# Kernel optimization log

Measured on AMD Instinct MI355X. Metric: run time of the kernel, lower is better.

The kernel has to match this reference:

```python
import jax, jax.numpy as jnp
import numpy as np

STRIDE = 1
PAD = 1
EXTENT = 3  # kernel footprint (ceil of max tap offset), 3x3 tap grid


def setup_inputs() -> dict:
    key = jax.random.key(0)
    k1, k2 = jax.random.split(key)
    B, Cin, H, W = 8, 64, 128, 128
    Cout, K = 64, 9
    x = jax.random.normal(k1, (B, Cin, H, W), dtype=jnp.float32)
    # per-tap weights, one scalar weight per (out_ch, in_ch, tap) -- op formula is 'x * w'
    weights = jax.random.normal(k2, (Cout, Cin, K), dtype=jnp.float32) * 0.05
    # 3x3 integer grid shifted by +0.4 -> non-integer offsets => bilinear (sub-pixel) gather
    base = jnp.stack(jnp.meshgrid(jnp.arange(3.0), jnp.arange(3.0), indexing='ij'), -1).reshape(9, 2)
    tap_offsets = (base + 0.4).astype(jnp.float32)  # [K, 2] (dy, dx)
    return {"x": x, "weights": weights, "tap_offsets": tap_offsets}


def _bilinear_tap(xp, dy, dx, H_out, W_out):
    # Gather xp at (oy*stride + dy, ox*stride + dx) with separable bilinear interp.
    Hp, Wp = xp.shape[-2], xp.shape[-1]
    y = jnp.arange(H_out, dtype=xp.dtype) * STRIDE + dy
    xc = jnp.arange(W_out, dtype=xp.dtype) * STRIDE + dx
    y0 = jnp.floor(y)
    x0 = jnp.floor(xc)
    fy = (y - y0)[None, None, :, None]
    fx = (xc - x0)[None, None, None, :]
    y0i = jnp.clip(y0.astype(jnp.int32), 0, Hp - 1)
    y1i = jnp.clip(y0.astype(jnp.int32) + 1, 0, Hp - 1)
    x0i = jnp.clip(x0.astype(jnp.int32), 0, Wp - 1)
    x1i = jnp.clip(x0.astype(jnp.int32) + 1, 0, Wp - 1)
    # interp rows first: [B, C, H_out, Wp]
    ry = xp[:, :, y0i, :] * (1.0 - fy) + xp[:, :, y1i, :] * fy
    # then columns: [B, C, H_out, W_out]
    return ry[:, :, :, x0i] * (1.0 - fx) + ry[:, :, :, x1i] * fx


def reference(x, weights, tap_offsets):
    B, Cin, H, W = x.shape
    K = weights.shape[-1]
    xp = jnp.pad(x, ((0, 0), (0, 0), (PAD, PAD), (PAD, PAD)))
    H_out = (H + 2 * PAD - EXTENT) // STRIDE + 1
    W_out = (W + 2 * PAD - EXTENT) // STRIDE + 1
    # gather all taps (loop over small fixed K=9, each fully vectorized over B,C,H,W)
    taps = [_bilinear_tap(xp, tap_offsets[k, 0], tap_offsets[k, 1], H_out, W_out)
            for k in range(K)]
    g = jnp.stack(taps, 0)  # [K, B, Cin, H_out, W_out]
    # per-tap op 'x * w', accumulated over taps and input channels
    return jnp.einsum('kbiyx,oik->boyx', g, weights)  # [B, Cout, H_out, W_out]
```

## Files before the change

kernel.cpp:

```cpp
#include <hip/hip_runtime.h>


#define CIN   64
#define COUT  64
#define HH    128
#define WW    128

typedef __attribute__((ext_vector_type(8))) short bf16x8;
typedef __attribute__((ext_vector_type(4))) float f32x4;
typedef __attribute__((ext_vector_type(4))) unsigned int u32x4;

__device__ __forceinline__ unsigned short f2bf(float f) {
  unsigned int u = __float_as_uint(f);
  u = (u + 0x7fffu + ((u >> 16) & 1u)) >> 16;
  return (unsigned short)u;
}

__global__ void make_wb(const float* __restrict__ wgt,
                        const float* __restrict__ off,
                        unsigned short* __restrict__ wb2)
{
  int id = blockIdx.x * 64 + threadIdx.x;
  int o = id >> 6, c = id & 63;
  float W16[16];
  #pragma unroll
  for (int i = 0; i < 16; ++i) W16[i] = 0.f;
  for (int k = 0; k < 9; ++k) {
    float dy = off[2*k], dx = off[2*k+1];
    float fyf = floorf(dy), fxf = floorf(dx);
    int   iy = (int)fyf,   ix = (int)fxf;
    float fy = dy - fyf,   fx = dx - fxf;
    float wk = wgt[(o*CIN + c)*9 + k];
    W16[(iy  )*4 + ix  ] += wk * (1.f-fy)*(1.f-fx);
    W16[(iy  )*4 + ix+1] += wk * (1.f-fy)*fx;
    W16[(iy+1)*4 + ix  ] += wk * fy*(1.f-fx);
    W16[(iy+1)*4 + ix+1] += wk * fy*fx;
  }
  int p = c >> 5, q = (c >> 3) & 3, j = c & 7;
  int n = o >> 4, m15 = o & 15;
  int lanei = q*16 + m15;
  for (int rs = 0; rs < 16; ++rs)
    wb2[(size_t)(((p*16 + rs)*4 + n)*64 + lanei)*8 + j] = f2bf(W16[rs]);
}

__global__ __launch_bounds__(128, 2)
void conv_mfma(const float* __restrict__ x,
               const unsigned short* __restrict__ wb2,
               float* __restrict__ out)
{
  __shared__ unsigned short tile[4 * 132 * 32];

  const int wg  = blockIdx.x;
  const int xcd = wg & 7;
  const int i8  = wg >> 3;
  const int b   = i8 >> 4;
  const int y0  = xcd * 16 + (i8 & 15);
  const int t    = threadIdx.x;
  const int wave = t >> 6;
  const int lane = t & 63;
  const int m15  = lane & 15;
  const int q    = lane >> 4;

  f32x4 acc[4][4];
  #pragma unroll
  for (int mi = 0; mi < 4; ++mi)
    #pragma unroll
    for (int n = 0; n < 4; ++n)
      acc[mi][n] = (f32x4){0.f, 0.f, 0.f, 0.f};

  #pragma unroll
  for (int p = 0; p < 2; ++p) {
    if (p) __syncthreads();

    if (p == 0) {
      int row = t >> 5, rem = t & 31;
      int csel = rem >> 3;
      int col  = (csel == 0) ? 0 : (128 + csel);
      int w8   = rem & 7;
      *(unsigned long long*)&tile[(row*132 + col)*32 + w8*4] = 0ull;
    }

    #pragma unroll 4
    for (int it = 0; it < 16; ++it) {
      int g     = it*2 + wave;
      int row   = g >> 3;
      int rem   = g & 7;
      int chunk = rem >> 1;
      int xh    = rem & 1;
      int px    = xh*64 + lane;
      int gy    = y0 + row - 1;
      unsigned int pk[4];
      if ((unsigned)gy < (unsigned)HH) {
        const float* ps = x + ((size_t)((b*CIN + p*32 + chunk*8)*HH + gy))*WW + px;
        float v[8];
        #pragma unroll
        for (int cc = 0; cc < 8; ++cc) v[cc] = ps[(size_t)cc*HH*WW];
        #pragma unroll
        for (int i = 0; i < 4; ++i)
          pk[i] = (unsigned int)f2bf(v[2*i]) | ((unsigned int)f2bf(v[2*i+1]) << 16);
      } else {
        pk[0] = pk[1] = pk[2] = pk[3] = 0u;
      }
      int pos  = px + 1;
      int slot = (chunk + (pos >> 2)) & 3;
      *(u32x4*)&tile[((row*132 + pos)*4 + slot)*8] = *(u32x4*)pk;
    }
    __syncthreads();

    const unsigned short* wstream = wb2 + (size_t)p*16*4*512 + lane*8;
    #pragma unroll
    for (int rs = 0; rs < 16; ++rs) {
      const int r = rs >> 2, s = rs & 3;
      bf16x8 bfr[4];
      #pragma unroll
      for (int n = 0; n < 4; ++n)
        bfr[n] = *(const bf16x8*)(wstream + (rs*4 + n)*512);
      bf16x8 afr[4];
      #pragma unroll
      for (int mi = 0; mi < 4; ++mi) {
        int pos  = wave*64 + mi*16 + m15 + s;
        int slot = (q + (pos >> 2)) & 3;
        afr[mi] = *(const bf16x8*)(&tile[((r*132 + pos)*4 + slot)*8]);
      }
      #pragma unroll
      for (int mi = 0; mi < 4; ++mi)
        #pragma unroll
        for (int n = 0; n < 4; ++n)
          acc[mi][n] = __builtin_amdgcn_mfma_f32_16x16x32_bf16(afr[mi], bfr[n], acc[mi][n], 0, 0, 0);
    }
  }

  __syncthreads();
  float* epi = (float*)tile;
  #pragma unroll
  for (int mi = 0; mi < 4; ++mi)
    #pragma unroll
    for (int n = 0; n < 4; ++n) {
      int o  = n*16 + m15;
      int px = wave*64 + mi*16 + q*4;
      *(f32x4*)&epi[o*132 + px] = acc[mi][n];
    }
  __syncthreads();
  #pragma unroll
  for (int i = 0; i < 16; ++i) {
    int o  = i*4 + (t >> 5);
    int px = (t & 31) * 4;
    f32x4 v = *(const f32x4*)&epi[o*132 + px];
    *(f32x4*)&out[(((size_t)(b*COUT + o))*HH + y0)*WW + px] = v;
  }
}

extern "C" void kernel_launch(void* const* d_in, const int* in_sizes, int n_in,
                              void* d_out, int out_size, void* d_ws, size_t ws_size,
                              hipStream_t stream)
{
  const float* x   = (const float*)d_in[0];
  const float* wgt = (const float*)d_in[1];
  const float* off = (const float*)d_in[2];
  float* out = (float*)d_out;
  unsigned short* wb2 = (unsigned short*)d_ws;

  make_wb<<<64, 64, 0, stream>>>(wgt, off, wb2);
  conv_mfma<<<1024, 128, 0, stream>>>(x, wb2, out);
}
```

Measured before the change: 107.2 us.

## Pre-pack input to swizzled bf16 and stream tiles via global_load_lds

Adds a prep kernel that converts x once into a channel-packed, pre-swizzled bf16 layout in workspace, fused with the weight folding. The conv kernel then copies rows straight into LDS with global_load_lds 16-byte transfers, with no per-element fp32 loads, conversion or repacking. This removes the redundant 3x row re-reads and conversions done per workgroup. In exchange it adds an extra full pass over x (read fp32, write bf16) and a larger workspace footprint.

```diff
diff --git a/kernel.cpp b/kernel.cpp
--- a/kernel.cpp
+++ b/kernel.cpp
@@ -10,41 +10,76 @@
 typedef __attribute__((ext_vector_type(4))) float f32x4;
 typedef __attribute__((ext_vector_type(4))) unsigned int u32x4;
 
+#define GLOBAL_AS __attribute__((address_space(1)))
+#define LDS_AS    __attribute__((address_space(3)))
+
 __device__ __forceinline__ unsigned short f2bf(float f) {
   unsigned int u = __float_as_uint(f);
   u = (u + 0x7fffu + ((u >> 16) & 1u)) >> 16;
   return (unsigned short)u;
 }
 
-__global__ void make_wb(const float* __restrict__ wgt,
-                        const float* __restrict__ off,
-                        unsigned short* __restrict__ wb2)
+#define NREPACK 512
+#define NWB     16
+
+__global__ void prep(const float* __restrict__ x,
+                     const float* __restrict__ wgt,
+                     const float* __restrict__ off,
+                     unsigned short* __restrict__ xb,
+                     unsigned short* __restrict__ wb2)
 {
-  int id = blockIdx.x * 64 + threadIdx.x;
-  int o = id >> 6, c = id & 63;
-  float W16[16];
-  #pragma unroll
-  for (int i = 0; i < 16; ++i) W16[i] = 0.f;
-  for (int k = 0; k < 9; ++k) {
-    float dy = off[2*k], dx = off[2*k+1];
-    float fyf = floorf(dy), fxf = floorf(dx);
-    int   iy = (int)fyf,   ix = (int)fxf;
-    float fy = dy - fyf,   fx = dx - fxf;
-    float wk = wgt[(o*CIN + c)*9 + k];
-    W16[(iy  )*4 + ix  ] += wk * (1.f-fy)*(1.f-fx);
-    W16[(iy  )*4 + ix+1] += wk * (1.f-fy)*fx;
-    W16[(iy+1)*4 + ix  ] += wk * fy*(1.f-fx);
-    W16[(iy+1)*4 + ix+1] += wk * fy*fx;
+  if (blockIdx.x < NREPACK) {
+    int id = blockIdx.x * 256 + threadIdx.x;
+    int px = id & 127;
+    int y  = (id >> 7) & 127;
+    int b  = id >> 14;
+    int q4 = ((px + 1) >> 2) & 3;
+    unsigned int pk[2][16];
+    #pragma unroll
+    for (int i = 0; i < 16; ++i) { pk[0][i] = 0u; pk[1][i] = 0u; }
+    const float* src = x + ((size_t)b*CIN*HH + y)*WW + px;
+    #pragma unroll
+    for (int c = 0; c < CIN; ++c) {
+      float v = src[(size_t)c*HH*WW];
+      int p = c >> 5, chunk = (c >> 3) & 3, j = c & 7;
+      pk[p][chunk*4 + (j >> 1)] |= (unsigned int)f2bf(v) << ((j & 1) * 16);
+    }
+    #pragma unroll
+    for (int p = 0; p < 2; ++p) {
+      unsigned short* dst = xb + (((size_t)(b*2 + p)*HH + y)*WW + px)*32;
+      #pragma unroll
+      for (int chunk = 0; chunk < 4; ++chunk) {
+        int slot = (chunk + q4) & 3;
+        *(u32x4*)(dst + slot*8) = *(u32x4*)&pk[p][chunk*4];
+      }
+    }
+  } else {
+    int id = (blockIdx.x - NREPACK) * 256 + threadIdx.x;
+    int o = id >> 6, c = id & 63;
+    float W16[16];
+    #pragma unroll
+    for (int i = 0; i < 16; ++i) W16[i] = 0.f;
+    for (int k = 0; k < 9; ++k) {
+      float dy = off[2*k], dx = off[2*k+1];
+      float fyf = floorf(dy), fxf = floorf(dx);
+      int   iy = (int)fyf,   ix = (int)fxf;
+      float fy = dy - fyf,   fx = dx - fxf;
+      float wk = wgt[(o*CIN + c)*9 + k];
+      W16[(iy  )*4 + ix  ] += wk * (1.f-fy)*(1.f-fx);
+      W16[(iy  )*4 + ix+1] += wk * (1.f-fy)*fx;
+      W16[(iy+1)*4 + ix  ] += wk * fy*(1.f-fx);
+      W16[(iy+1)*4 + ix+1] += wk * fy*fx;
+    }
+    int p = c >> 5, q = (c >> 3) & 3, j = c & 7;
+    int n = o >> 4, m15 = o & 15;
+    int lanei = q*16 + m15;
+    for (int rs = 0; rs < 16; ++rs)
+      wb2[(size_t)(((p*16 + rs)*4 + n)*64 + lanei)*8 + j] = f2bf(W16[rs]);
   }
-  int p = c >> 5, q = (c >> 3) & 3, j = c & 7;
-  int n = o >> 4, m15 = o & 15;
-  int lanei = q*16 + m15;
-  for (int rs = 0; rs < 16; ++rs)
-    wb2[(size_t)(((p*16 + rs)*4 + n)*64 + lanei)*8 + j] = f2bf(W16[rs]);
 }
 
 __global__ __launch_bounds__(128, 2)
-void conv_mfma(const float* __restrict__ x,
+void conv_mfma(const unsigned short* __restrict__ xb,
                const unsigned short* __restrict__ wb2,
                float* __restrict__ out)
 {
@@ -68,6 +103,8 @@
     for (int n = 0; n < 4; ++n)
       acc[mi][n] = (f32x4){0.f, 0.f, 0.f, 0.f};
 
+  const size_t rowstride = (size_t)WW * 32;
+
   #pragma unroll
   for (int p = 0; p < 2; ++p) {
     if (p) __syncthreads();
@@ -80,30 +117,21 @@
       *(unsigned long long*)&tile[(row*132 + col)*32 + w8*4] = 0ull;
     }
 
-    #pragma unroll 4
+    const unsigned short* xbase = xb + (size_t)(b*2 + p)*HH*rowstride;
+    #pragma unroll
     for (int it = 0; it < 16; ++it) {
-      int g     = it*2 + wave;
-      int row   = g >> 3;
-      int rem   = g & 7;
-      int chunk = rem >> 1;
-      int xh    = rem & 1;
-      int px    = xh*64 + lane;
-      int gy    = y0 + row - 1;
-      unsigned int pk[4];
+      int g   = it*2 + wave;
+      int row = g >> 3;
+      int seg = g & 7;
+      int gy  = y0 + row - 1;
+      unsigned short* ldsdst = &tile[(row*132 + 1)*32 + seg*512];
       if ((unsigned)gy < (unsigned)HH) {
-        const float* ps = x + ((size_t)((b*CIN + p*32 + chunk*8)*HH + gy))*WW + px;
-        float v[8];
-        #pragma unroll
-        for (int cc = 0; cc < 8; ++cc) v[cc] = ps[(size_t)cc*HH*WW];
-        #pragma unroll
-        for (int i = 0; i < 4; ++i)
-          pk[i] = (unsigned int)f2bf(v[2*i]) | ((unsigned int)f2bf(v[2*i+1]) << 16);
-      } else {
-        pk[0] = pk[1] = pk[2] = pk[3] = 0u;
+        const unsigned short* src = xbase + (size_t)gy*rowstride + seg*512 + lane*8;
+        __builtin_amdgcn_global_load_lds((const GLOBAL_AS unsigned int*)src,
+                                         (LDS_AS unsigned int*)ldsdst, 16, 0, 0);
+      } else if (p == 0) {
+        *(u32x4*)(ldsdst + lane*8) = (u32x4){0u,0u,0u,0u};
       }
-      int pos  = px + 1;
-      int slot = (chunk + (pos >> 2)) & 3;
-      *(u32x4*)&tile[((row*132 + pos)*4 + slot)*8] = *(u32x4*)pk;
     }
     __syncthreads();
 
@@ -159,7 +187,8 @@
   const float* off = (const float*)d_in[2];
   float* out = (float*)d_out;
   unsigned short* wb2 = (unsigned short*)d_ws;
+  unsigned short* xb  = (unsigned short*)d_ws + 65536;
 
-  make_wb<<<64, 64, 0, stream>>>(wgt, off, wb2);
-  conv_mfma<<<1024, 128, 0, stream>>>(x, wb2, out);
+  prep<<<NREPACK + NWB, 256, 0, stream>>>(x, wgt, off, xb, wb2);
+  conv_mfma<<<1024, 128, 0, stream>>>(xb, wb2, out);
 }
```

Result: slower. 113.2 us (+5.7%).

## Compute two output rows per block with 4 waves sharing a 5-row input tile

Applied to the files above, without the earlier changes.

Each workgroup now produces two adjacent output rows with 256 threads: waves split by output row and by output-channel half, and they share a 5-row staged input tile instead of two separate 4-row tiles. This cuts redundant global loads and bf16 conversion of the overlapping input rows and halves the number of blocks. Halo rows are zeroed only on the first pass, and the epilogue writes the two rows in turn through shared memory using nontemporal stores. In exchange, per-wave accumulators grow to 8x2 MFMA tiles, the epilogue needs extra barriers, and half as many blocks may lower occupancy.

```diff
diff --git a/kernel.cpp b/kernel.cpp
--- a/kernel.cpp
+++ b/kernel.cpp
@@ -43,36 +43,39 @@
     wb2[(size_t)(((p*16 + rs)*4 + n)*64 + lanei)*8 + j] = f2bf(W16[rs]);
 }
 
-__global__ __launch_bounds__(128, 2)
+__global__ __launch_bounds__(256, 2)
 void conv_mfma(const float* __restrict__ x,
                const unsigned short* __restrict__ wb2,
                float* __restrict__ out)
 {
-  __shared__ unsigned short tile[4 * 132 * 32];
+  __shared__ unsigned short tile[5 * 132 * 32];
 
   const int wg  = blockIdx.x;
   const int xcd = wg & 7;
-  const int i8  = wg >> 3;
-  const int b   = i8 >> 4;
-  const int y0  = xcd * 16 + (i8 & 15);
-  const int t    = threadIdx.x;
-  const int wave = t >> 6;
-  const int lane = t & 63;
-  const int m15  = lane & 15;
-  const int q    = lane >> 4;
+  const int i   = wg >> 3;
+  const int b   = i >> 3;
+  const int ss  = i & 7;
+  const int y0  = xcd * 16 + ss * 2;
+  const int t     = threadIdx.x;
+  const int wave  = t >> 6;
+  const int lane  = t & 63;
+  const int m15   = lane & 15;
+  const int q     = lane >> 4;
+  const int yr    = wave >> 1;
+  const int ohalf = wave & 1;
 
-  f32x4 acc[4][4];
+  f32x4 acc[8][2];
   #pragma unroll
-  for (int mi = 0; mi < 4; ++mi)
+  for (int mi = 0; mi < 8; ++mi)
     #pragma unroll
-    for (int n = 0; n < 4; ++n)
-      acc[mi][n] = (f32x4){0.f, 0.f, 0.f, 0.f};
+    for (int nn = 0; nn < 2; ++nn)
+      acc[mi][nn] = (f32x4){0.f, 0.f, 0.f, 0.f};
 
   #pragma unroll
   for (int p = 0; p < 2; ++p) {
     if (p) __syncthreads();
 
-    if (p == 0) {
+    if (p == 0 && t < 160) {
       int row = t >> 5, rem = t & 31;
       int csel = rem >> 3;
       int col  = (csel == 0) ? 0 : (128 + csel);
@@ -80,73 +83,79 @@
       *(unsigned long long*)&tile[(row*132 + col)*32 + w8*4] = 0ull;
     }
 
-    #pragma unroll 4
-    for (int it = 0; it < 16; ++it) {
-      int g     = it*2 + wave;
+    #pragma unroll 2
+    for (int it = 0; it < 10; ++it) {
+      int g     = it*4 + wave;
       int row   = g >> 3;
       int rem   = g & 7;
       int chunk = rem >> 1;
       int xh    = rem & 1;
       int px    = xh*64 + lane;
       int gy    = y0 + row - 1;
-      unsigned int pk[4];
+      int pos   = px + 1;
+      int slot  = (chunk + (pos >> 2)) & 3;
       if ((unsigned)gy < (unsigned)HH) {
         const float* ps = x + ((size_t)((b*CIN + p*32 + chunk*8)*HH + gy))*WW + px;
         float v[8];
         #pragma unroll
         for (int cc = 0; cc < 8; ++cc) v[cc] = ps[(size_t)cc*HH*WW];
+        unsigned int pk[4];
         #pragma unroll
-        for (int i = 0; i < 4; ++i)
-          pk[i] = (unsigned int)f2bf(v[2*i]) | ((unsigned int)f2bf(v[2*i+1]) << 16);
-      } else {
-        pk[0] = pk[1] = pk[2] = pk[3] = 0u;
+        for (int ii = 0; ii < 4; ++ii)
+          pk[ii] = (unsigned int)f2bf(v[2*ii]) | ((unsigned int)f2bf(v[2*ii+1]) << 16);
+        *(u32x4*)&tile[((row*132 + pos)*4 + slot)*8] = *(u32x4*)pk;
+      } else if (p == 0) {
+        *(u32x4*)&tile[((row*132 + pos)*4 + slot)*8] = (u32x4){0u,0u,0u,0u};
       }
-      int pos  = px + 1;
-      int slot = (chunk + (pos >> 2)) & 3;
-      *(u32x4*)&tile[((row*132 + pos)*4 + slot)*8] = *(u32x4*)pk;
     }
     __syncthreads();
 
-    const unsigned short* wstream = wb2 + (size_t)p*16*4*512 + lane*8;
+    const unsigned short* wstream = wb2 + (size_t)p*32768 + lane*8;
     #pragma unroll
     for (int rs = 0; rs < 16; ++rs) {
       const int r = rs >> 2, s = rs & 3;
-      bf16x8 bfr[4];
+      bf16x8 bfr[2];
       #pragma unroll
-      for (int n = 0; n < 4; ++n)
-        bfr[n] = *(const bf16x8*)(wstream + (rs*4 + n)*512);
-      bf16x8 afr[4];
+      for (int nn = 0; nn < 2; ++nn)
+        bfr[nn] = *(const bf16x8*)(wstream + (rs*4 + ohalf*2 + nn)*512);
+      bf16x8 afr[8];
       #pragma unroll
-      for (int mi = 0; mi < 4; ++mi) {
-        int pos  = wave*64 + mi*16 + m15 + s;
+      for (int mi = 0; mi < 8; ++mi) {
+        int pos  = mi*16 + m15 + s;
         int slot = (q + (pos >> 2)) & 3;
-        afr[mi] = *(const bf16x8*)(&tile[((r*132 + pos)*4 + slot)*8]);
+        afr[mi] = *(const bf16x8*)(&tile[(((yr + r)*132 + pos)*4 + slot)*8]);
       }
       #pragma unroll
-      for (int mi = 0; mi < 4; ++mi)
+      for (int mi = 0; mi < 8; ++mi)
         #pragma unroll
-        for (int n = 0; n < 4; ++n)
-          acc[mi][n] = __builtin_amdgcn_mfma_f32_16x16x32_bf16(afr[mi], bfr[n], acc[mi][n], 0, 0, 0);
+        for (int nn = 0; nn < 2; ++nn)
+          acc[mi][nn] = __builtin_amdgcn_mfma_f32_16x16x32_bf16(afr[mi], bfr[nn], acc[mi][nn], 0, 0, 0);
     }
   }
 
-  __syncthreads();
   float* epi = (float*)tile;
   #pragma unroll
-  for (int mi = 0; mi < 4; ++mi)
+  for (int yr2 = 0; yr2 < 2; ++yr2) {
+    __syncthreads();
+    if (yr == yr2) {
+      #pragma unroll
+      for (int mi = 0; mi < 8; ++mi)
+        #pragma unroll
+        for (int nn = 0; nn < 2; ++nn) {
+          int o  = (ohalf*2 + nn)*16 + m15;
+          int px = mi*16 + q*4;
+          *(f32x4*)&epi[o*132 + px] = acc[mi][nn];
+        }
+    }
+    __syncthreads();
     #pragma unroll
-    for (int n = 0; n < 4; ++n) {
-      int o  = n*16 + m15;
-      int px = wave*64 + mi*16 + q*4;
-      *(f32x4*)&epi[o*132 + px] = acc[mi][n];
+    for (int ii = 0; ii < 8; ++ii) {
+      int o  = ii*8 + (t >> 5);
+      int px = (t & 31) * 4;
+      f32x4 v = *(const f32x4*)&epi[o*132 + px];
+      __builtin_nontemporal_store(v,
+          (f32x4*)&out[(((size_t)(b*COUT + o))*HH + (y0 + yr2))*WW + px]);
     }
-  __syncthreads();
-  #pragma unroll
-  for (int i = 0; i < 16; ++i) {
-    int o  = i*4 + (t >> 5);
-    int px = (t & 31) * 4;
-    f32x4 v = *(const f32x4*)&epi[o*132 + px];
-    *(f32x4*)&out[(((size_t)(b*COUT + o))*HH + y0)*WW + px] = v;
   }
 }
 
@@ -161,5 +170,5 @@
   unsigned short* wb2 = (unsigned short*)d_ws;
 
   make_wb<<<64, 64, 0, stream>>>(wgt, off, wb2);
-  conv_mfma<<<1024, 128, 0, stream>>>(x, wb2, out);
+  conv_mfma<<<512, 256, 0, stream>>>(x, wb2, out);
 }
```

Result: slower. 119.7 us (+11.7%).

## Split output rows into half-width tiles and split Cout across waves

Applied to the files above, without the earlier changes.

Each workgroup now covers a 64-pixel half row instead of a full 128-pixel row, doubling the grid to 2048 blocks. The two waves now split output channels (32 each) rather than pixels, which halves the accumulator registers per wave, and launch bounds are raised to allow 4 blocks per CU. The goal is more occupancy and a smaller LDS tile. The cost is redundant halo loads (66 of 64 columns plus the extra input rows) and each wave reading the full A tile.

```diff
diff --git a/kernel.cpp b/kernel.cpp
--- a/kernel.cpp
+++ b/kernel.cpp
@@ -5,6 +5,7 @@
 #define COUT  64
 #define HH    128
 #define WW    128
+#define NC    68
 
 typedef __attribute__((ext_vector_type(8))) short bf16x8;
 typedef __attribute__((ext_vector_type(4))) float f32x4;
@@ -43,90 +44,104 @@
     wb2[(size_t)(((p*16 + rs)*4 + n)*64 + lanei)*8 + j] = f2bf(W16[rs]);
 }
 
-__global__ __launch_bounds__(128, 2)
+__global__ __launch_bounds__(128, 4)
 void conv_mfma(const float* __restrict__ x,
                const unsigned short* __restrict__ wb2,
                float* __restrict__ out)
 {
-  __shared__ unsigned short tile[4 * 132 * 32];
+  __shared__ __align__(16) unsigned short tile[4 * NC * 32];
 
   const int wg  = blockIdx.x;
   const int xcd = wg & 7;
-  const int i8  = wg >> 3;
-  const int b   = i8 >> 4;
-  const int y0  = xcd * 16 + (i8 & 15);
+  const int i   = wg >> 3;
+  const int b   = i >> 5;
+  const int r5  = i & 31;
+  const int y0  = xcd * 16 + (r5 >> 1);
+  const int x0  = (r5 & 1) * 64;
   const int t    = threadIdx.x;
   const int wave = t >> 6;
   const int lane = t & 63;
   const int m15  = lane & 15;
   const int q    = lane >> 4;
 
-  f32x4 acc[4][4];
+  f32x4 acc[4][2];
   #pragma unroll
   for (int mi = 0; mi < 4; ++mi)
     #pragma unroll
-    for (int n = 0; n < 4; ++n)
-      acc[mi][n] = (f32x4){0.f, 0.f, 0.f, 0.f};
+    for (int nn = 0; nn < 2; ++nn)
+      acc[mi][nn] = (f32x4){0.f, 0.f, 0.f, 0.f};
 
   #pragma unroll
   for (int p = 0; p < 2; ++p) {
     if (p) __syncthreads();
 
-    if (p == 0) {
-      int row = t >> 5, rem = t & 31;
-      int csel = rem >> 3;
-      int col  = (csel == 0) ? 0 : (128 + csel);
-      int w8   = rem & 7;
-      *(unsigned long long*)&tile[(row*132 + col)*32 + w8*4] = 0ull;
-    }
+    #pragma unroll
+    for (int it = 0; it < 8; ++it) {
+      int g     = it*2 + wave;
+      int row   = g >> 2;
+      int chunk = g & 3;
+      int gy    = y0 + row - 1;
 
-    #pragma unroll 4
-    for (int it = 0; it < 16; ++it) {
-      int g     = it*2 + wave;
-      int row   = g >> 3;
-      int rem   = g & 7;
-      int chunk = rem >> 1;
-      int xh    = rem & 1;
-      int px    = xh*64 + lane;
-      int gy    = y0 + row - 1;
-      unsigned int pk[4];
-      if ((unsigned)gy < (unsigned)HH) {
-        const float* ps = x + ((size_t)((b*CIN + p*32 + chunk*8)*HH + gy))*WW + px;
-        float v[8];
-        #pragma unroll
-        for (int cc = 0; cc < 8; ++cc) v[cc] = ps[(size_t)cc*HH*WW];
-        #pragma unroll
-        for (int i = 0; i < 4; ++i)
-          pk[i] = (unsigned int)f2bf(v[2*i]) | ((unsigned int)f2bf(v[2*i+1]) << 16);
-      } else {
-        pk[0] = pk[1] = pk[2] = pk[3] = 0u;
+      {
+        int gx   = x0 - 1 + lane;
+        int slot = (chunk + (lane >> 2)) & 3;
+        unsigned short* dst = &tile[((row*NC + lane)*4 + slot)*8];
+        if (((unsigned)gy < (unsigned)HH) && ((unsigned)gx < (unsigned)WW)) {
+          const float* ps = x + ((size_t)(b*CIN + p*32 + chunk*8)*HH + gy)*WW + gx;
+          float v[8];
+          #pragma unroll
+          for (int cc = 0; cc < 8; ++cc) v[cc] = ps[(size_t)cc*HH*WW];
+          unsigned int pk[4];
+          #pragma unroll
+          for (int ii = 0; ii < 4; ++ii)
+            pk[ii] = (unsigned int)f2bf(v[2*ii]) | ((unsigned int)f2bf(v[2*ii+1]) << 16);
+          *(u32x4*)dst = *(u32x4*)pk;
+        } else if (p == 0) {
+          *(u32x4*)dst = (u32x4){0u,0u,0u,0u};
+        }
       }
-      int pos  = px + 1;
-      int slot = (chunk + (pos >> 2)) & 3;
-      *(u32x4*)&tile[((row*132 + pos)*4 + slot)*8] = *(u32x4*)pk;
+      if (lane < 3) {
+        int col  = 64 + lane;
+        int gx   = x0 + 63 + lane;
+        int slot = (chunk + (col >> 2)) & 3;
+        unsigned short* dst = &tile[((row*NC + col)*4 + slot)*8];
+        if (((unsigned)gy < (unsigned)HH) && ((unsigned)gx < (unsigned)WW)) {
+          const float* ps = x + ((size_t)(b*CIN + p*32 + chunk*8)*HH + gy)*WW + gx;
+          float v[8];
+          #pragma unroll
+          for (int cc = 0; cc < 8; ++cc) v[cc] = ps[(size_t)cc*HH*WW];
+          unsigned int pk[4];
+          #pragma unroll
+          for (int ii = 0; ii < 4; ++ii)
+            pk[ii] = (unsigned int)f2bf(v[2*ii]) | ((unsigned int)f2bf(v[2*ii+1]) << 16);
+          *(u32x4*)dst = *(u32x4*)pk;
+        } else if (p == 0) {
+          *(u32x4*)dst = (u32x4){0u,0u,0u,0u};
+        }
+      }
     }
     __syncthreads();
 
-    const unsigned short* wstream = wb2 + (size_t)p*16*4*512 + lane*8;
+    const unsigned short* wstream = wb2 + (size_t)p*32768 + (size_t)lane*8;
     #pragma unroll
     for (int rs = 0; rs < 16; ++rs) {
       const int r = rs >> 2, s = rs & 3;
-      bf16x8 bfr[4];
+      bf16x8 bfr[2];
       #pragma unroll
-      for (int n = 0; n < 4; ++n)
-        bfr[n] = *(const bf16x8*)(wstream + (rs*4 + n)*512);
+      for (int nn = 0; nn < 2; ++nn)
+        bfr[nn] = *(const bf16x8*)(wstream + (rs*4 + wave*2 + nn)*512);
       bf16x8 afr[4];
       #pragma unroll
       for (int mi = 0; mi < 4; ++mi) {
-        int pos  = wave*64 + mi*16 + m15 + s;
-        int slot = (q + (pos >> 2)) & 3;
-        afr[mi] = *(const bf16x8*)(&tile[((r*132 + pos)*4 + slot)*8]);
+        int c    = mi*16 + m15 + s;
+        int slot = (q + (c >> 2)) & 3;
+        afr[mi] = *(const bf16x8*)&tile[((r*NC + c)*4 + slot)*8];
       }
       #pragma unroll
       for (int mi = 0; mi < 4; ++mi)
         #pragma unroll
-        for (int n = 0; n < 4; ++n)
-          acc[mi][n] = __builtin_amdgcn_mfma_f32_16x16x32_bf16(afr[mi], bfr[n], acc[mi][n], 0, 0, 0);
+        for (int nn = 0; nn < 2; ++nn)
+          acc[mi][nn] = __builtin_amdgcn_mfma_f32_16x16x32_bf16(afr[mi], bfr[nn], acc[mi][nn], 0, 0, 0);
     }
   }
 
@@ -135,18 +150,18 @@
   #pragma unroll
   for (int mi = 0; mi < 4; ++mi)
     #pragma unroll
-    for (int n = 0; n < 4; ++n) {
-      int o  = n*16 + m15;
-      int px = wave*64 + mi*16 + q*4;
-      *(f32x4*)&epi[o*132 + px] = acc[mi][n];
+    for (int nn = 0; nn < 2; ++nn) {
+      int o  = (wave*2 + nn)*16 + m15;
+      int px = mi*16 + q*4;
+      *(f32x4*)&epi[o*NC + px] = acc[mi][nn];
     }
   __syncthreads();
   #pragma unroll
-  for (int i = 0; i < 16; ++i) {
-    int o  = i*4 + (t >> 5);
-    int px = (t & 31) * 4;
-    f32x4 v = *(const f32x4*)&epi[o*132 + px];
-    *(f32x4*)&out[(((size_t)(b*COUT + o))*HH + y0)*WW + px] = v;
+  for (int round = 0; round < 8; ++round) {
+    int idx = round*512 + t*4;
+    int o = idx >> 6, px = idx & 63;
+    f32x4 v = *(const f32x4*)&epi[o*NC + px];
+    *(f32x4*)&out[(((size_t)(b*COUT + o))*HH + y0)*WW + x0 + px] = v;
   }
 }
 
@@ -161,5 +176,5 @@
   unsigned short* wb2 = (unsigned short*)d_ws;
 
   make_wb<<<64, 64, 0, stream>>>(wgt, off, wb2);
-  conv_mfma<<<1024, 128, 0, stream>>>(x, wb2, out);
+  conv_mfma<<<2048, 128, 0, stream>>>(x, wb2, out);
 }
```

Result: slower. 117.9 us (+10.0%).
